# Performance work log

Measured on AMD Instinct MI355X. Metric: run time of the kernel, lower is better.

Reference implementation:

```python
import jax, jax.numpy as jnp
import numpy as np

NUM_HEADS = 16

def setup_inputs() -> dict:
    key = jax.random.key(0)
    ks = jax.random.split(key, 8)
    B, S, D = 2, 2048, 1024
    H = NUM_HEADS
    s = 0.02
    return {
        "x": jax.random.normal(ks[0], (B, S, D), jnp.float32),
        "Wqkv": jax.random.normal(ks[1], (D, 3 * D), jnp.float32) * s,
        "bqkv": jnp.zeros((3 * D,), jnp.float32),
        "Wo": jax.random.normal(ks[2], (D, D), jnp.float32) * s,
        "bo": jnp.zeros((D,), jnp.float32),
        "mobius_scale": jnp.full((H,), 0.1, jnp.float32),
        "W1": jax.random.normal(ks[3], (D, D // 2), jnp.float32) * s,
        "b1": jnp.zeros((D // 2,), jnp.float32),
        "W2": jax.random.normal(ks[4], (D // 2, H), jnp.float32) * s,
        "b2": jnp.zeros((H,), jnp.float32),
        "adaptive_weight": jnp.full((1,), 0.1, jnp.float32),
    }

def reference(x, Wqkv, bqkv, Wo, bo, mobius_scale, W1, b1, W2, b2, adaptive_weight):
    B, S, D = x.shape
    H = NUM_HEADS
    dh = D // H
    # --- adaptive gating MLP on pooled context ---
    context = jnp.mean(x, axis=1, keepdims=True)                      # (B,1,D)
    h = jax.nn.gelu(context @ W1 + b1, approximate=False)             # (B,1,D/2)
    adaptive_factors = jax.nn.sigmoid(h @ W2 + b2)                    # (B,1,H)
    # --- incidence attention with mobius term ---
    qkv = (x @ Wqkv + bqkv).reshape(B, S, 3, H, dh)
    q, k, v = qkv[:, :, 0], qkv[:, :, 1], qkv[:, :, 2]                # (B,S,H,dh)
    scores = jnp.einsum("bshd,bthd->bhst", q, k) / jnp.sqrt(jnp.float32(dh))
    # Mobius map of the raw scores, learnable per-head scale
    scores = scores + mobius_scale[None, :, None, None] * (scores / (1.0 + scores * scores))
    attn = jax.nn.softmax(scores, axis=-1)                            # (B,H,S,S)
    out = jnp.einsum("bhst,bthd->bshd", attn, v).reshape(B, S, D)
    base_output = out @ Wo + bo                                       # (B,S,D)
    # --- training-path elementwise rescale ---
    adjustment = jnp.mean(adaptive_factors, axis=-1, keepdims=True)   # (B,1,1)
    return base_output * (1.0 + adaptive_weight * adjustment)
```

## Files before the change

### kernel.cpp

```cpp
#include <hip/hip_runtime.h>
#include <hip/hip_bf16.h>
#include <stdint.h>

typedef unsigned short u16;
typedef unsigned int u32;
typedef __attribute__((ext_vector_type(8))) short short8;
typedef __attribute__((ext_vector_type(4))) float f32x4;
typedef __attribute__((ext_vector_type(2))) float f32x2;
typedef __attribute__((ext_vector_type(4))) unsigned short u16x4;
typedef __attribute__((ext_vector_type(2))) unsigned int u32x2;

#define DEVFN static __device__ __forceinline__


DEVFN u16 f2bf(float f) {
  u32 u = __float_as_uint(f);
  u = (u + 0x7FFFu + ((u >> 16) & 1u)) >> 16;
  return (u16)u;
}

DEVFN u32 cvtpk_bf16(float lo, float hi) {
  u32 r;
  asm("v_cvt_pk_bf16_f32 %0, %1, %2" : "=v"(r) : "v"(lo), "v"(hi));
  return r;
}

DEVFN void gll16(const void* g, void* l) {
  __builtin_amdgcn_global_load_lds((const __attribute__((address_space(1))) u32*)g,
                                   (__attribute__((address_space(3))) u32*)l, 16, 0, 0);
}

__global__ void ctx_cvt_kernel(const float* __restrict__ x, float* __restrict__ ctx,
                               u16* __restrict__ xbf) {
  int blk = blockIdx.x;
  int b = blk >> 7;
  int s0 = (blk & 127) * 16;
  int t = threadIdx.x;
  const float* xb = x + ((size_t)b * 2048 + s0) * 1024 + t * 4;
  u16* ob = xbf + ((size_t)b * 2048 + s0) * 1024 + t * 4;
  float4 sum = {0.f, 0.f, 0.f, 0.f};
#pragma unroll
  for (int s = 0; s < 16; ++s) {
    float4 v = *(const float4*)(xb + (size_t)s * 1024);
    sum.x += v.x;
    sum.y += v.y;
    sum.z += v.z;
    sum.w += v.w;
    u16x4 o = {f2bf(v.x), f2bf(v.y), f2bf(v.z), f2bf(v.w)};
    *(u16x4*)(ob + (size_t)s * 1024) = o;
  }
  float* c = ctx + b * 1024 + t * 4;
  atomicAdd(c + 0, sum.x);
  atomicAdd(c + 1, sum.y);
  atomicAdd(c + 2, sum.z);
  atomicAdd(c + 3, sum.w);
}

__global__ void adaptive1_kernel(const float* __restrict__ ctx, const float* __restrict__ W1,
                                 const float* __restrict__ b1, float* __restrict__ hbuf) {
  int b = blockIdx.x >> 4, jq = blockIdx.x & 15;
  int t = threadIdx.x;
  int jl = t & 31, dp = t >> 5;
  int j = jq * 32 + jl;
  __shared__ float ctxs[1024];
  __shared__ float partial[8][32];
  for (int i = t; i < 1024; i += 256) ctxs[i] = ctx[b * 1024 + i] * (1.0f / 2048.0f);
  __syncthreads();
  float a0 = 0.f, a1 = 0.f;
  int d0 = dp * 128;
  for (int d = d0; d < d0 + 128; d += 2) {
    a0 += ctxs[d] * W1[(size_t)d * 512 + j];
    a1 += ctxs[d + 1] * W1[(size_t)(d + 1) * 512 + j];
  }
  partial[dp][jl] = a0 + a1;
  __syncthreads();
  if (t < 32) {
    float acc = b1[jq * 32 + t];
#pragma unroll
    for (int p = 0; p < 8; ++p) acc += partial[p][t];
    hbuf[b * 512 + jq * 32 + t] =
        0.5f * acc * (1.0f + erff(acc * 0.70710678118654752f));
  }
}

__global__ void adaptive2_kernel(const float* __restrict__ hbuf, const float* __restrict__ W2,
                                 const float* __restrict__ b2, const float* __restrict__ aw,
                                 float* __restrict__ scale) {
  int b = blockIdx.x;
  int t = threadIdx.x;
  __shared__ float part[256];
  int o = t & 15, seg = t >> 4;
  float a = 0.f;
  for (int j = seg * 32; j < seg * 32 + 32; ++j) a += hbuf[b * 512 + j] * W2[(size_t)j * 16 + o];
  part[t] = a;
  __syncthreads();
  if (t < 16) {
    float acc = b2[t];
    for (int s2 = 0; s2 < 16; ++s2) acc += part[s2 * 16 + t];
    part[t] = 1.0f / (1.0f + __expf(-acc));
  }
  __syncthreads();
  if (t == 0) {
    float s = 0.f;
    for (int i = 0; i < 16; ++i) s += part[i];
    scale[b] = 1.0f + aw[0] * (s * (1.0f / 16.0f));
  }
}

__global__ void transpose_bf16_kernel(const float* __restrict__ in, u16* __restrict__ out,
                                      int K, int N) {
  __shared__ u16 tile[32][33];
  int n0 = blockIdx.x * 32, k0 = blockIdx.y * 32;
  int tc = threadIdx.x & 31, tr = threadIdx.x >> 5;
  for (int i = tr; i < 32; i += 8)
    tile[i][tc] = f2bf(in[(size_t)(k0 + i) * N + n0 + tc]);
  __syncthreads();
  for (int i = tr; i < 32; i += 8)
    out[(size_t)(n0 + i) * K + k0 + tc] = tile[tc][i];
}


DEVFN void gemm_tile_mainloop(const u16* __restrict__ A, const u16* __restrict__ Bt,
                              int m0, int n0, int K, u16* As, u16* Bs, f32x4 acc[4][4]) {
  const int tid = threadIdx.x;
  const int lane = tid & 63, wid = tid >> 6;
  const int wr = wid >> 1, wc = wid & 1;
  const int lr = lane & 15, lg = lane >> 4;
  const int srow = tid >> 2;
  const int scol = ((tid & 3) ^ ((tid >> 3) & 3)) * 8;
  const int axor = ((lr >> 1) & 3) << 4;

  const u16* ag0 = A + (size_t)(m0 + srow) * K + scol;
  const u16* ag1 = ag0 + (size_t)64 * K;
  const u16* bg0 = Bt + (size_t)(n0 + srow) * K + scol;
  const u16* bg1 = bg0 + (size_t)64 * K;

  gll16(ag0, As + tid * 8);
  gll16(ag1, As + (tid + 256) * 8);
  gll16(bg0, Bs + tid * 8);
  gll16(bg1, Bs + (tid + 256) * 8);

  int cur = 0;
  for (int k0 = 0; k0 < K; k0 += 32) {
    __syncthreads();
    if (k0 + 32 < K) {
      int nb = (cur ^ 1) * 4096;
      gll16(ag0 + k0 + 32, As + nb + tid * 8);
      gll16(ag1 + k0 + 32, As + nb + (tid + 256) * 8);
      gll16(bg0 + k0 + 32, Bs + nb + tid * 8);
      gll16(bg1 + k0 + 32, Bs + nb + (tid + 256) * 8);
    }
    const char* Ac = (const char*)(As + cur * 4096);
    const char* Bc = (const char*)(Bs + cur * 4096);
    short8 af[4], bf[4];
#pragma unroll
    for (int i = 0; i < 4; ++i)
      af[i] = *(const short8*)(Ac + (wr * 64 + i * 16 + lr) * 64 + ((lg * 16) ^ axor));
#pragma unroll
    for (int j = 0; j < 4; ++j)
      bf[j] = *(const short8*)(Bc + (wc * 64 + j * 16 + lr) * 64 + ((lg * 16) ^ axor));
#pragma unroll
    for (int i = 0; i < 4; ++i)
#pragma unroll
      for (int j = 0; j < 4; ++j)
        acc[i][j] = __builtin_amdgcn_mfma_f32_16x16x32_bf16(bf[j], af[i], acc[i][j], 0, 0, 0);
    cur ^= 1;
  }
}

DEVFN void gemm64_mainloop(const u16* __restrict__ A, const u16* __restrict__ Bt,
                           int m0, int n0, int K, u16* As, u16* Bs, f32x4 acc[2][2]) {
  const int tid = threadIdx.x;
  const int lane = tid & 63, wid = tid >> 6;
  const int wr = wid >> 1, wc = wid & 1;
  const int lr = lane & 15, lg = lane >> 4;
  const int srow = tid >> 2;
  const int scol = ((tid & 3) ^ ((tid >> 3) & 3)) * 8;
  const int axor = ((lr >> 1) & 3) << 4;

  const u16* ag = A + (size_t)(m0 + srow) * K + scol;
  const u16* bg = Bt + (size_t)(n0 + srow) * K + scol;
  gll16(ag, As + tid * 8);
  gll16(bg, Bs + tid * 8);

  int cur = 0;
  for (int k0 = 0; k0 < K; k0 += 32) {
    __syncthreads();
    if (k0 + 32 < K) {
      int nb = (cur ^ 1) * 2048;
      gll16(ag + k0 + 32, As + nb + tid * 8);
      gll16(bg + k0 + 32, Bs + nb + tid * 8);
    }
    const char* Ac = (const char*)(As + cur * 2048);
    const char* Bc = (const char*)(Bs + cur * 2048);
    short8 af[2], bf[2];
#pragma unroll
    for (int i = 0; i < 2; ++i)
      af[i] = *(const short8*)(Ac + (wr * 32 + i * 16 + lr) * 64 + ((lg * 16) ^ axor));
#pragma unroll
    for (int j = 0; j < 2; ++j)
      bf[j] = *(const short8*)(Bc + (wc * 32 + j * 16 + lr) * 64 + ((lg * 16) ^ axor));
#pragma unroll
    for (int i = 0; i < 2; ++i)
#pragma unroll
      for (int j = 0; j < 2; ++j)
        acc[i][j] = __builtin_amdgcn_mfma_f32_16x16x32_bf16(bf[j], af[i], acc[i][j], 0, 0, 0);
    cur ^= 1;
  }
}

__global__ __launch_bounds__(256) void gemm_qkv_kernel(
    const u16* __restrict__ A, const u16* __restrict__ Bt, const float* __restrict__ bias,
    u16* __restrict__ Qb, u16* __restrict__ Kb, u16* __restrict__ Vt) {
  __shared__ __align__(16) u16 As[2 * 128 * 32];
  __shared__ __align__(16) u16 Bs[2 * 128 * 32];
  f32x4 acc[4][4];
  const f32x4 z = {0.f, 0.f, 0.f, 0.f};
#pragma unroll
  for (int i = 0; i < 4; ++i)
#pragma unroll
    for (int j = 0; j < 4; ++j) acc[i][j] = z;
  int lin = blockIdx.x;
  int swz = (lin & 7) * 96 + (lin >> 3);
  int n0 = (swz % 24) * 128, m0 = (swz / 24) * 128;
  gemm_tile_mainloop(A, Bt, m0, n0, 1024, As, Bs, acc);

  const int lane = threadIdx.x & 63, wid = threadIdx.x >> 6;
  const int wr = wid >> 1, wc = wid & 1, lr = lane & 15, lg = lane >> 4;
#pragma unroll
  for (int i = 0; i < 4; ++i) {
    int m = m0 + wr * 64 + i * 16 + lr;
#pragma unroll
    for (int j = 0; j < 4; ++j) {
      int nb = n0 + wc * 64 + j * 16 + lg * 4;
      float4 bv = *(const float4*)&bias[nb];
      int c3 = nb >> 10;
      if (c3 == 2) {
        int bb = m >> 11, ss = m & 2047;
        int hh = (nb >> 6) & 15, dd = nb & 63;
        size_t vb_ = (((size_t)bb * 16 + hh) * 64 + dd) * 2048 + ss;
        Vt[vb_] = f2bf(acc[i][j][0] + bv.x);
        Vt[vb_ + 2048] = f2bf(acc[i][j][1] + bv.y);
        Vt[vb_ + 4096] = f2bf(acc[i][j][2] + bv.z);
        Vt[vb_ + 6144] = f2bf(acc[i][j][3] + bv.w);
      } else {
        u16* dst = (c3 == 0) ? Qb : Kb;
        float qs = (c3 == 0) ? 0.125f : 1.0f;
        u16x4 o = {f2bf((acc[i][j][0] + bv.x) * qs), f2bf((acc[i][j][1] + bv.y) * qs),
                   f2bf((acc[i][j][2] + bv.z) * qs), f2bf((acc[i][j][3] + bv.w) * qs)};
        *(u16x4*)&dst[(size_t)m * 1024 + (nb & 1023)] = o;
      }
    }
  }
}

__global__ __launch_bounds__(256) void gemm_out_kernel(
    const u16* __restrict__ A, const u16* __restrict__ Bt, const float* __restrict__ bo,
    const float* __restrict__ scale, float* __restrict__ out) {
  __shared__ __align__(16) u16 As[2 * 64 * 32];
  __shared__ __align__(16) u16 Bs[2 * 64 * 32];
  f32x4 acc[2][2];
  const f32x4 z = {0.f, 0.f, 0.f, 0.f};
#pragma unroll
  for (int i = 0; i < 2; ++i)
#pragma unroll
    for (int j = 0; j < 2; ++j) acc[i][j] = z;
  int lin = blockIdx.x;
  int swz = (lin & 7) * 128 + (lin >> 3);
  int n0 = (swz & 15) * 64, m0 = (swz >> 4) * 64;
  gemm64_mainloop(A, Bt, m0, n0, 1024, As, Bs, acc);

  const int lane = threadIdx.x & 63, wid = threadIdx.x >> 6;
  const int wr = wid >> 1, wc = wid & 1, lr = lane & 15, lg = lane >> 4;
#pragma unroll
  for (int i = 0; i < 2; ++i) {
    int m = m0 + wr * 32 + i * 16 + lr;
    float sc = scale[m >> 11];
#pragma unroll
    for (int j = 0; j < 2; ++j) {
      int nb = n0 + wc * 32 + j * 16 + lg * 4;
      float4 bv = *(const float4*)&bo[nb];
      float4 o = {(acc[i][j][0] + bv.x) * sc, (acc[i][j][1] + bv.y) * sc,
                  (acc[i][j][2] + bv.z) * sc, (acc[i][j][3] + bv.w) * sc};
      *(float4*)&out[(size_t)m * 1024 + nb] = o;
    }
  }
}

__global__ __launch_bounds__(256) void attn_kernel(
    const u16* __restrict__ Qb, const u16* __restrict__ Kb, const u16* __restrict__ Vt,
    const float* __restrict__ mobius, u16* __restrict__ O) {
  __shared__ __align__(16) u16 Ks[2][64 * 64];
  __shared__ __align__(16) u16 Vs[2][64 * 64];
  __shared__ __align__(16) u16 Ps[64 * 64];
  const int tid = threadIdx.x;
  const int lane = tid & 63, w = tid >> 6;
  const int lr = lane & 15, lg = lane >> 4;
  const int bid = blockIdx.x;
  const int bidx = (bid & 7) * 128 + (bid >> 3);
  const int qb = bidx & 31, h = (bidx >> 5) & 15, b = bidx >> 9;
  const float msc = mobius[h];

  const int srow = tid >> 3;
  const int scol = ((tid & 7) ^ (srow & 7)) * 8;
  const int rxor = (lr & 7) << 4;

  const u16* qgl = Qb + (size_t)(b * 2048 + qb * 64 + w * 16 + lr) * 1024 + h * 64 + lg * 8;
  short8 qf0 = *(const short8*)qgl;
  short8 qf1 = *(const short8*)(qgl + 32);

  const u16* kg = Kb + (size_t)(b * 2048 + srow) * 1024 + h * 64 + scol;
  const u16* vg = Vt + ((size_t)(b * 16 + h) * 64 + srow) * 2048 + scol;

  gll16(kg, Ks[0] + tid * 8);
  gll16(kg + (size_t)32 * 1024, Ks[0] + (tid + 256) * 8);
  gll16(vg, Vs[0] + tid * 8);
  gll16(vg + 32 * 2048, Vs[0] + (tid + 256) * 8);

  float m_run = -3.0e38f, l_run = 0.0f;
  f32x4 acc_o[4];
  const f32x4 z = {0.f, 0.f, 0.f, 0.f};
#pragma unroll
  for (int i = 0; i < 4; ++i) acc_o[i] = z;

  const float L2E = 1.44269504f;
  const f32x2 one2 = {1.0f, 1.0f};
  const f32x2 msc2 = {msc, msc};
  const f32x2 l2e2 = {L2E, L2E};
  const int qrow = w * 16 + lr;
  const char* Pc = (const char*)Ps;
  int cur = 0;
  for (int kt = 0; kt < 32; ++kt) {
    __syncthreads();
    if (kt < 31) {
      const u16* kgn = kg + (size_t)(kt + 1) * 64 * 1024;
      const u16* vgn = vg + (kt + 1) * 64;
      u16* Kn = Ks[cur ^ 1];
      u16* Vn = Vs[cur ^ 1];
      gll16(kgn, Kn + tid * 8);
      gll16(kgn + (size_t)32 * 1024, Kn + (tid + 256) * 8);
      gll16(vgn, Vn + tid * 8);
      gll16(vgn + 32 * 2048, Vn + (tid + 256) * 8);
    }
    const char* Kc = (const char*)Ks[cur];
    const char* Vc = (const char*)Vs[cur];

    f32x4 sacc[4];
#pragma unroll
    for (int i = 0; i < 4; ++i) sacc[i] = z;
    __builtin_amdgcn_s_setprio(1);
    {
      int cbx = (lg * 16) ^ rxor;
#pragma unroll
      for (int ki = 0; ki < 4; ++ki) {
        short8 kf = *(const short8*)(Kc + (ki * 16 + lr) * 128 + cbx);
        sacc[ki] = __builtin_amdgcn_mfma_f32_16x16x32_bf16(kf, qf0, sacc[ki], 0, 0, 0);
      }
      cbx = (64 + lg * 16) ^ rxor;
#pragma unroll
      for (int ki = 0; ki < 4; ++ki) {
        short8 kf = *(const short8*)(Kc + (ki * 16 + lr) * 128 + cbx);
        sacc[ki] = __builtin_amdgcn_mfma_f32_16x16x32_bf16(kf, qf1, sacc[ki], 0, 0, 0);
      }
    }
    __builtin_amdgcn_s_setprio(0);

    f32x2 p2[8];
    f32x2 mx = {-3.0e38f, -3.0e38f};
#pragma unroll
    for (int i = 0; i < 8; ++i) {
      int ki = i >> 1, jj = i & 1;
      f32x2 s = {sacc[ki][jj * 2], sacc[ki][jj * 2 + 1]};
      f32x2 d = s * s + one2;
      f32x2 rr = {__builtin_amdgcn_rcpf(d.x), __builtin_amdgcn_rcpf(d.y)};
      f32x2 tl = (msc2 * (s * rr) + s) * l2e2;
      p2[i] = tl;
      mx = __builtin_elementwise_max(mx, tl);
    }
    float tmax = fmaxf(mx.x, mx.y);
    tmax = fmaxf(tmax, __shfl_xor(tmax, 16));
    tmax = fmaxf(tmax, __shfl_xor(tmax, 32));
    if (__any(tmax > m_run + 8.0f)) {
      float m_new = fmaxf(m_run, tmax);
      float corr = __builtin_amdgcn_exp2f(m_run - m_new);
      m_run = m_new;
      l_run *= corr;
#pragma unroll
      for (int di = 0; di < 4; ++di)
#pragma unroll
        for (int r = 0; r < 4; ++r) acc_o[di][r] *= corr;
    }
    f32x2 m2 = {m_run, m_run};
    f32x2 sum2 = {0.f, 0.f};
#pragma unroll
    for (int i = 0; i < 8; ++i) {
      f32x2 e = p2[i] - m2;
      f32x2 pe = {__builtin_amdgcn_exp2f(e.x), __builtin_amdgcn_exp2f(e.y)};
      p2[i] = pe;
      sum2 += pe;
    }
    float tsum = sum2.x + sum2.y;
    tsum += __shfl_xor(tsum, 16);
    tsum += __shfl_xor(tsum, 32);
    l_run += tsum;

#pragma unroll
    for (int ki = 0; ki < 4; ++ki) {
      u32x2 pw = {cvtpk_bf16(p2[2 * ki].x, p2[2 * ki].y),
                  cvtpk_bf16(p2[2 * ki + 1].x, p2[2 * ki + 1].y)};
      *(u32x2*)(Pc + qrow * 128 + ((ki * 32 + lg * 8) ^ rxor)) = pw;
    }

    __builtin_amdgcn_s_setprio(1);
#pragma unroll
    for (int ks = 0; ks < 2; ++ks) {
      int cbx = (ks * 64 + lg * 16) ^ rxor;
      short8 pf = *(const short8*)(Pc + qrow * 128 + cbx);
#pragma unroll
      for (int di = 0; di < 4; ++di) {
        short8 vf = *(const short8*)(Vc + (di * 16 + lr) * 128 + cbx);
        acc_o[di] = __builtin_amdgcn_mfma_f32_16x16x32_bf16(vf, pf, acc_o[di], 0, 0, 0);
      }
    }
    __builtin_amdgcn_s_setprio(0);
    cur ^= 1;
  }

  float linv = 1.0f / l_run;
  size_t obase = ((size_t)(b * 2048 + qb * 64 + w * 16 + lr)) * 1024 + h * 64;
#pragma unroll
  for (int di = 0; di < 4; ++di) {
    u32x2 o = {cvtpk_bf16(acc_o[di][0] * linv, acc_o[di][1] * linv),
               cvtpk_bf16(acc_o[di][2] * linv, acc_o[di][3] * linv)};
    *(u32x2*)&O[obase + di * 16 + lg * 4] = o;
  }
}


extern "C" void kernel_launch(void* const* d_in, const int* in_sizes, int n_in,
                              void* d_out, int out_size, void* d_ws, size_t ws_size,
                              hipStream_t stream) {
  const float* x = (const float*)d_in[0];
  const float* Wqkv = (const float*)d_in[1];
  const float* bqkv = (const float*)d_in[2];
  const float* Wo = (const float*)d_in[3];
  const float* bo = (const float*)d_in[4];
  const float* mob = (const float*)d_in[5];
  const float* W1 = (const float*)d_in[6];
  const float* b1 = (const float*)d_in[7];
  const float* W2 = (const float*)d_in[8];
  const float* b2 = (const float*)d_in[9];
  const float* aw = (const float*)d_in[10];
  float* out = (float*)d_out;

  const size_t MB = 1024 * 1024;
  char* ws = (char*)d_ws;
  float* scale = (float*)ws;
  float* ctx = (float*)(ws + 256);
  float* hbuf = (float*)(ws + 16384);
  char* base = ws + 32768;
  u16* xbf = (u16*)base;
  u16* wqkvT = (u16*)(base + 8 * MB);
  u16* woT = (u16*)(base + 14 * MB);
  u16* Qb = (u16*)(base + 16 * MB);
  u16* Kb = (u16*)(base + 24 * MB);
  u16* Vt = (u16*)(base + 32 * MB);
  u16* attn = (u16*)(base + 40 * MB);

  hipMemsetAsync(ctx, 0, 2048 * sizeof(float), stream);
  ctx_cvt_kernel<<<256, 256, 0, stream>>>(x, ctx, xbf);
  adaptive1_kernel<<<32, 256, 0, stream>>>(ctx, W1, b1, hbuf);
  adaptive2_kernel<<<2, 256, 0, stream>>>(hbuf, W2, b2, aw, scale);
  transpose_bf16_kernel<<<dim3(96, 32), 256, 0, stream>>>(Wqkv, wqkvT, 1024, 3072);
  transpose_bf16_kernel<<<dim3(32, 32), 256, 0, stream>>>(Wo, woT, 1024, 1024);
  gemm_qkv_kernel<<<768, 256, 0, stream>>>(xbf, wqkvT, bqkv, Qb, Kb, Vt);
  attn_kernel<<<1024, 256, 0, stream>>>(Qb, Kb, Vt, mob, attn);
  gemm_out_kernel<<<1024, 256, 0, stream>>>(attn, woT, bo, scale, out);
}
```

Before: 264.2 us.

## Split attention key tiles across wave pairs with end-of-loop softmax merge

```diff
diff --git a/kernel.cpp b/kernel.cpp
--- a/kernel.cpp
+++ b/kernel.cpp
@@ -287,14 +287,16 @@
   }
 }
 
-__global__ __launch_bounds__(256) void attn_kernel(
+__global__ __launch_bounds__(512, 6) void attn_kernel(
     const u16* __restrict__ Qb, const u16* __restrict__ Kb, const u16* __restrict__ Vt,
     const float* __restrict__ mobius, u16* __restrict__ O) {
-  __shared__ __align__(16) u16 Ks[2][64 * 64];
-  __shared__ __align__(16) u16 Vs[2][64 * 64];
-  __shared__ __align__(16) u16 Ps[64 * 64];
+  __shared__ __align__(16) char smem[40960];
+  u16* Ks = (u16*)smem;
+  u16* Vs = (u16*)(smem + 16384);
+  u16* Ps = (u16*)(smem + 32768);
   const int tid = threadIdx.x;
   const int lane = tid & 63, w = tid >> 6;
+  const int qg = w >> 1, half = w & 1;
   const int lr = lane & 15, lg = lane >> 4;
   const int bid = blockIdx.x;
   const int bidx = (bid & 7) * 128 + (bid >> 3);
@@ -305,17 +307,15 @@
   const int scol = ((tid & 7) ^ (srow & 7)) * 8;
   const int rxor = (lr & 7) << 4;
 
-  const u16* qgl = Qb + (size_t)(b * 2048 + qb * 64 + w * 16 + lr) * 1024 + h * 64 + lg * 8;
+  const u16* qgl = Qb + (size_t)(b * 2048 + qb * 64 + qg * 16 + lr) * 1024 + h * 64 + lg * 8;
   short8 qf0 = *(const short8*)qgl;
   short8 qf1 = *(const short8*)(qgl + 32);
 
   const u16* kg = Kb + (size_t)(b * 2048 + srow) * 1024 + h * 64 + scol;
   const u16* vg = Vt + ((size_t)(b * 16 + h) * 64 + srow) * 2048 + scol;
 
-  gll16(kg, Ks[0] + tid * 8);
-  gll16(kg + (size_t)32 * 1024, Ks[0] + (tid + 256) * 8);
-  gll16(vg, Vs[0] + tid * 8);
-  gll16(vg + 32 * 2048, Vs[0] + (tid + 256) * 8);
+  gll16(kg, Ks + tid * 8);
+  gll16(vg, Vs + tid * 8);
 
   float m_run = -3.0e38f, l_run = 0.0f;
   f32x4 acc_o[4];
@@ -327,50 +327,40 @@
   const f32x2 one2 = {1.0f, 1.0f};
   const f32x2 msc2 = {msc, msc};
   const f32x2 l2e2 = {L2E, L2E};
-  const int qrow = w * 16 + lr;
+  const int ki0 = half * 2;
+  const int qrow = qg * 16 + lr;
   const char* Pc = (const char*)Ps;
   int cur = 0;
   for (int kt = 0; kt < 32; ++kt) {
     __syncthreads();
     if (kt < 31) {
-      const u16* kgn = kg + (size_t)(kt + 1) * 64 * 1024;
-      const u16* vgn = vg + (kt + 1) * 64;
-      u16* Kn = Ks[cur ^ 1];
-      u16* Vn = Vs[cur ^ 1];
-      gll16(kgn, Kn + tid * 8);
-      gll16(kgn + (size_t)32 * 1024, Kn + (tid + 256) * 8);
-      gll16(vgn, Vn + tid * 8);
-      gll16(vgn + 32 * 2048, Vn + (tid + 256) * 8);
-    }
-    const char* Kc = (const char*)Ks[cur];
-    const char* Vc = (const char*)Vs[cur];
-
-    f32x4 sacc[4];
-#pragma unroll
-    for (int i = 0; i < 4; ++i) sacc[i] = z;
+      int nb = (cur ^ 1) * 4096;
+      gll16(kg + (size_t)(kt + 1) * 64 * 1024, Ks + nb + tid * 8);
+      gll16(vg + (kt + 1) * 64, Vs + nb + tid * 8);
+    }
+    const char* Kc = (const char*)(Ks + cur * 4096);
+    const char* Vc = (const char*)(Vs + cur * 4096);
+
+    f32x4 sacc[2];
+#pragma unroll
+    for (int i = 0; i < 2; ++i) sacc[i] = z;
     __builtin_amdgcn_s_setprio(1);
-    {
-      int cbx = (lg * 16) ^ rxor;
-#pragma unroll
-      for (int ki = 0; ki < 4; ++ki) {
-        short8 kf = *(const short8*)(Kc + (ki * 16 + lr) * 128 + cbx);
-        sacc[ki] = __builtin_amdgcn_mfma_f32_16x16x32_bf16(kf, qf0, sacc[ki], 0, 0, 0);
-      }
-      cbx = (64 + lg * 16) ^ rxor;
-#pragma unroll
-      for (int ki = 0; ki < 4; ++ki) {
-        short8 kf = *(const short8*)(Kc + (ki * 16 + lr) * 128 + cbx);
-        sacc[ki] = __builtin_amdgcn_mfma_f32_16x16x32_bf16(kf, qf1, sacc[ki], 0, 0, 0);
-      }
+#pragma unroll
+    for (int kk = 0; kk < 2; ++kk) {
+      int krow = (ki0 + kk) * 16 + lr;
+      short8 kfa = *(const short8*)(Kc + krow * 128 + ((lg * 16) ^ rxor));
+      sacc[kk] = __builtin_amdgcn_mfma_f32_16x16x32_bf16(kfa, qf0, sacc[kk], 0, 0, 0);
+      short8 kfb = *(const short8*)(Kc + krow * 128 + ((64 + lg * 16) ^ rxor));
+      sacc[kk] = __builtin_amdgcn_mfma_f32_16x16x32_bf16(kfb, qf1, sacc[kk], 0, 0, 0);
     }
     __builtin_amdgcn_s_setprio(0);
 
-    f32x2 p2[8];
+    f32x2 p2[4];
     f32x2 mx = {-3.0e38f, -3.0e38f};
 #pragma unroll
-    for (int i = 0; i < 8; ++i) {
-      int ki = i >> 1, jj = i & 1;
-      f32x2 s = {sacc[ki][jj * 2], sacc[ki][jj * 2 + 1]};
+    for (int i = 0; i < 4; ++i) {
+      int kk = i >> 1, jj = i & 1;
+      f32x2 s = {sacc[kk][jj * 2], sacc[kk][jj * 2 + 1]};
       f32x2 d = s * s + one2;
       f32x2 rr = {__builtin_amdgcn_rcpf(d.x), __builtin_amdgcn_rcpf(d.y)};
       f32x2 tl = (msc2 * (s * rr) + s) * l2e2;
@@ -393,7 +383,7 @@
     f32x2 m2 = {m_run, m_run};
     f32x2 sum2 = {0.f, 0.f};
 #pragma unroll
-    for (int i = 0; i < 8; ++i) {
+    for (int i = 0; i < 4; ++i) {
       f32x2 e = p2[i] - m2;
       f32x2 pe = {__builtin_amdgcn_exp2f(e.x), __builtin_amdgcn_exp2f(e.y)};
       p2[i] = pe;
@@ -405,16 +395,15 @@
     l_run += tsum;
 
 #pragma unroll
-    for (int ki = 0; ki < 4; ++ki) {
-      u32x2 pw = {cvtpk_bf16(p2[2 * ki].x, p2[2 * ki].y),
-                  cvtpk_bf16(p2[2 * ki + 1].x, p2[2 * ki + 1].y)};
-      *(u32x2*)(Pc + qrow * 128 + ((ki * 32 + lg * 8) ^ rxor)) = pw;
+    for (int kk = 0; kk < 2; ++kk) {
+      u32x2 pw = {cvtpk_bf16(p2[2 * kk].x, p2[2 * kk].y),
+                  cvtpk_bf16(p2[2 * kk + 1].x, p2[2 * kk + 1].y)};
+      *(u32x2*)(Pc + qrow * 128 + (((ki0 + kk) * 32 + lg * 8) ^ rxor)) = pw;
     }
 
     __builtin_amdgcn_s_setprio(1);
-#pragma unroll
-    for (int ks = 0; ks < 2; ++ks) {
-      int cbx = (ks * 64 + lg * 16) ^ rxor;
+    {
+      int cbx = (half * 64 + lg * 16) ^ rxor;
       short8 pf = *(const short8*)(Pc + qrow * 128 + cbx);
 #pragma unroll
       for (int di = 0; di < 4; ++di) {
@@ -426,13 +415,35 @@
     cur ^= 1;
   }
 
-  float linv = 1.0f / l_run;
-  size_t obase = ((size_t)(b * 2048 + qb * 64 + w * 16 + lr)) * 1024 + h * 64;
-#pragma unroll
-  for (int di = 0; di < 4; ++di) {
-    u32x2 o = {cvtpk_bf16(acc_o[di][0] * linv, acc_o[di][1] * linv),
-               cvtpk_bf16(acc_o[di][2] * linv, acc_o[di][3] * linv)};
-    *(u32x2*)&O[obase + di * 16 + lg * 4] = o;
+  __syncthreads();
+  float* xch = (float*)smem;
+  if (half) {
+    float* dst = xch + ((qg * 64) + lane) * 18;
+#pragma unroll
+    for (int di = 0; di < 4; ++di)
+#pragma unroll
+      for (int r = 0; r < 4; ++r) dst[di * 4 + r] = acc_o[di][r];
+    dst[16] = m_run;
+    dst[17] = l_run;
+  }
+  __syncthreads();
+  if (!half) {
+    const float* src = xch + ((qg * 64) + lane) * 18;
+    float m1 = src[16], l1 = src[17];
+    float m01 = fmaxf(m_run, m1);
+    float a0 = __builtin_amdgcn_exp2f(m_run - m01);
+    float a1 = __builtin_amdgcn_exp2f(m1 - m01);
+    float linv = 1.0f / (l_run * a0 + l1 * a1);
+    size_t obase = ((size_t)(b * 2048 + qb * 64 + qg * 16 + lr)) * 1024 + h * 64;
+#pragma unroll
+    for (int di = 0; di < 4; ++di) {
+      float o0 = (acc_o[di][0] * a0 + src[di * 4 + 0] * a1) * linv;
+      float o1 = (acc_o[di][1] * a0 + src[di * 4 + 1] * a1) * linv;
+      float o2 = (acc_o[di][2] * a0 + src[di * 4 + 2] * a1) * linv;
+      float o3 = (acc_o[di][3] * a0 + src[di * 4 + 3] * a1) * linv;
+      u32x2 o = {cvtpk_bf16(o0, o1), cvtpk_bf16(o2, o3)};
+      *(u32x2*)&O[obase + di * 16 + lg * 4] = o;
+    }
   }
 }
 
@@ -474,6 +485,6 @@
   transpose_bf16_kernel<<<dim3(96, 32), 256, 0, stream>>>(Wqkv, wqkvT, 1024, 3072);
   transpose_bf16_kernel<<<dim3(32, 32), 256, 0, stream>>>(Wo, woT, 1024, 1024);
   gemm_qkv_kernel<<<768, 256, 0, stream>>>(xbf, wqkvT, bqkv, Qb, Kb, Vt);
-  attn_kernel<<<1024, 256, 0, stream>>>(Qb, Kb, Vt, mob, attn);
+  attn_kernel<<<1024, 512, 0, stream>>>(Qb, Kb, Vt, mob, attn);
   gemm_out_kernel<<<1024, 256, 0, stream>>>(attn, woT, bo, scale, out);
 }
```

After: 260.0 us. Within noise of the previous version (-1.6%).
